# Kernel optimization log

Measured on AMD Instinct MI355X. Metric: run time of the kernel, lower is better.

## Reference

```python
import jax, jax.numpy as jnp
import numpy as np

# Analytic closed form of the 4-qubit circuit. Wires (0,1) and (2,3) are
# independent 2-qubit blocks: RY(x_a)oRY(x_b) -> CNOT(a,b) -> RY(p_a)oRY(p_b).
# Heisenberg picture gives:
#   <Z_a> = cos(p_a)*cos(x_a) + sin(p_a)*sin(x_a)*sin(x_b)
#   <Z_b> = cos(p_b)*cos(x_a)*cos(x_b) + sin(p_b)*sin(x_b)

def setup_inputs() -> dict:
    key = jax.random.key(0)
    k1, k2, k3, k4 = jax.random.split(key, 4)
    B = 16384
    return {
        "x": jax.random.uniform(k1, (B, 1, 28, 28), dtype=jnp.float32),
        "vqc_params": jax.random.normal(k2, (4,), dtype=jnp.float32),
        "fc_w": jax.random.normal(k3, (10, 784), dtype=jnp.float32) * 0.05,
        "fc_b": jax.random.normal(k4, (10,), dtype=jnp.float32) * 0.05,
        "bias": jnp.zeros((10,), dtype=jnp.float32),
    }


def _pair_expvals(xa, xb, pa, pb):
    # xa, xb: [B, 196]; pa, pb: scalars
    za = jnp.cos(pa) * jnp.cos(xa) + jnp.sin(pa) * jnp.sin(xa) * jnp.sin(xb)
    zb = jnp.cos(pb) * jnp.cos(xa) * jnp.cos(xb) + jnp.sin(pb) * jnp.sin(xb)
    return za, zb


def reference(x, vqc_params, fc_w, fc_b, bias):
    B = x.shape[0]
    # Extract 2x2 patches in the same (r, c) row-major order as the torch loop.
    # [B,28,28] -> [B,14,2,14,2] -> [B,14,14,2,2] -> [B,196,4]
    p = x[:, 0].reshape(B, 14, 2, 14, 2).transpose(0, 1, 3, 2, 4).reshape(B, 196, 4)
    x0, x1, x2, x3 = p[..., 0], p[..., 1], p[..., 2], p[..., 3]
    p0, p1, p2, p3 = vqc_params[0], vqc_params[1], vqc_params[2], vqc_params[3]
    z0, z1 = _pair_expvals(x0, x1, p0, p1)
    z2, z3 = _pair_expvals(x2, x3, p2, p3)
    q = jnp.stack([z0, z1, z2, z3], axis=-1).reshape(B, 4 * 196)  # patch-major, wire-minor
    logits = q @ fc_w.T + fc_b - bias
    return jax.nn.log_softmax(logits, axis=-1)
```

## Files before the change

### kernel.cpp

```cpp
#include <hip/hip_runtime.h>


typedef __attribute__((ext_vector_type(8))) short short8;
typedef __attribute__((ext_vector_type(4))) float f32x4;

constexpr int BLOCK = 512;
constexpr int IMGS  = 16;
constexpr int S2    = 808;
constexpr int NIT   = 4;

static __device__ __forceinline__ unsigned pkbf2(float lo, float hi) {
    unsigned r;
    asm("v_cvt_pk_bf16_f32 %0, %1, %2" : "=v"(r) : "v"(lo), "v"(hi));
    return r;
}

__global__ __launch_bounds__(BLOCK, 6)
void quanv_mfma(const float* __restrict__ x,
                const float* __restrict__ vqc,
                const float* __restrict__ fc_w,
                const float* __restrict__ fc_b,
                const float* __restrict__ bias,
                float* __restrict__ out,
                int B)
{
    __shared__ __align__(16) unsigned short q_lds[IMGS * S2];

    const int tid  = threadIdx.x;
    const int lane = tid & 63;
    const int wv   = tid >> 6;
    const int i16  = lane & 15;
    const int g    = lane >> 4;
    const int imgBase = blockIdx.x * IMGS;

    float S0, C0, S1, C1, S2p, C2p, S3, C3;
    __sincosf(vqc[0], &S0, &C0);
    __sincosf(vqc[1], &S1, &C1);
    __sincosf(vqc[2], &S2p, &C2p);
    __sincosf(vqc[3], &S3, &C3);

    if (tid < 192) {
        const unsigned im = (unsigned)tid / 12u;
        const unsigned o  = (unsigned)tid - 12u * im;
        *reinterpret_cast<unsigned*>(&q_lds[im * S2 + 784 + 2 * o]) = 0u;
    }

    const float4* __restrict__ xf4 =
        reinterpret_cast<const float4*>(x) + (long)imgBase * 196;

    unsigned img = (unsigned)tid / 196u;
    unsigned jv  = (unsigned)tid - 196u * img;

    auto process = [&](float4 v, unsigned im, unsigned j) {
        const unsigned y   = (j * 1171u) >> 13;
        const unsigned cx  = j - 7u * y;
        const unsigned par = y & 1u;
        const float CA = par ? C2p : C0, SA = par ? S2p : S0;
        const float CB = par ? C3  : C1, SB = par ? S3  : S1;
        float sa, ca, sb, cb;
        __sincosf(v.x, &sa, &ca);  __sincosf(v.y, &sb, &cb);
        const float za1 = CA * ca + SA * (sa * sb);
        const float zb1 = CB * (ca * cb) + SB * sb;
        __sincosf(v.z, &sa, &ca);  __sincosf(v.w, &sb, &cb);
        const float za2 = CA * ca + SA * (sa * sb);
        const float zb2 = CB * (ca * cb) + SB * sb;
        const unsigned e = im * S2 + (y >> 1) * 56u + 8u * cx + 2u * par;
        *reinterpret_cast<unsigned*>(&q_lds[e])     = pkbf2(za1, zb1);
        *reinterpret_cast<unsigned*>(&q_lds[e + 4]) = pkbf2(za2, zb2);
    };

    #pragma unroll
    for (int bt = 0; bt < 2; ++bt) {
        const float4 r0 = xf4[(bt * 3 + 0) * BLOCK + tid];
        const float4 r1 = xf4[(bt * 3 + 1) * BLOCK + tid];
        const float4 r2 = xf4[(bt * 3 + 2) * BLOCK + tid];
        process(r0, img, jv);
        img += 2; jv += 120; if (jv >= 196) { jv -= 196; img += 1; }
        process(r1, img, jv);
        img += 2; jv += 120; if (jv >= 196) { jv -= 196; img += 1; }
        process(r2, img, jv);
        img += 2; jv += 120; if (jv >= 196) { jv -= 196; img += 1; }
    }
    if (tid < 64) {
        const float4 r = xf4[6 * BLOCK + tid];
        process(r, img, jv);
    }

    __syncthreads();

    const int ncl = (i16 < 10) ? i16 : 9;
    const float* __restrict__ wrow = fc_w + ncl * 784;
    short8 bf[NIT];
    #pragma unroll
    for (int I = 0; I < NIT; ++I) {
        const int kb = wv + 8 * I;
        if (kb < 25) {
            int k = kb * 32 + 8 * g;
            if (k > 776) k = 776;
            const float4 lo4 = *reinterpret_cast<const float4*>(wrow + k);
            const float4 hi4 = *reinterpret_cast<const float4*>(wrow + k + 4);
            union { unsigned u[4]; short8 s; } t;
            t.u[0] = pkbf2(lo4.x, lo4.y);
            t.u[1] = pkbf2(lo4.z, lo4.w);
            t.u[2] = pkbf2(hi4.x, hi4.y);
            t.u[3] = pkbf2(hi4.z, hi4.w);
            bf[I] = t.s;
        }
    }

    f32x4 acc = {0.f, 0.f, 0.f, 0.f};
    #pragma unroll
    for (int I = 0; I < NIT; ++I) {
        const int kb = wv + 8 * I;
        if (kb < 25) {
            const short8 a = *reinterpret_cast<const short8*>(
                &q_lds[i16 * S2 + kb * 32 + 8 * g]);
            acc = __builtin_amdgcn_mfma_f32_16x16x32_bf16(a, bf[I], acc, 0, 0, 0);
        }
    }

    __syncthreads();
    float* const cpart = reinterpret_cast<float*>(q_lds);
    if (wv > 0)
        *reinterpret_cast<f32x4*>(&cpart[(wv - 1) * 256 + lane * 4]) = acc;
    __syncthreads();

    if (wv == 0) {
        #pragma unroll
        for (int p = 0; p < 7; ++p)
            acc += *reinterpret_cast<const f32x4*>(&cpart[p * 256 + lane * 4]);
        const float bk = (i16 < 10) ? (fc_b[i16] - bias[i16]) : 0.f;

        #pragma unroll
        for (int r = 0; r < 4; ++r) {
            const float lg = acc[r] + bk;
            float mx = (i16 < 10) ? lg : -3.0e38f;
            #pragma unroll
            for (int off = 1; off < 16; off <<= 1)
                mx = fmaxf(mx, __shfl_xor(mx, off, 64));
            float s = (i16 < 10) ? __expf(lg - mx) : 0.f;
            #pragma unroll
            for (int off = 1; off < 16; off <<= 1)
                s += __shfl_xor(s, off, 64);
            const int im = imgBase + g * 4 + r;
            if (i16 < 10 && im < B)
                out[(long)im * 10 + i16] = lg - mx - __logf(s);
        }
    }
}

extern "C" void kernel_launch(void* const* d_in, const int* in_sizes, int n_in,
                              void* d_out, int out_size, void* d_ws, size_t ws_size,
                              hipStream_t stream) {
    const float* x    = (const float*)d_in[0];
    const float* vqc  = (const float*)d_in[1];
    const float* fc_w = (const float*)d_in[2];
    const float* fc_b = (const float*)d_in[3];
    const float* bias = (const float*)d_in[4];
    float* outp = (float*)d_out;

    const int B = in_sizes[0] / 784;
    const int nblocks = (B + IMGS - 1) / IMGS;
    hipLaunchKernelGGL(quanv_mfma, dim3(nblocks), dim3(BLOCK), 0, stream,
                       x, vqc, fc_w, fc_b, bias, outp, B);
}
```

Baseline: 17.61 us.

## Process two image slabs per block with register prefetch of the next slab

Each block now handles two 16-image slabs in sequence, loading the second slab's pixels into registers while the first slab's MFMA and softmax run. The fc weights are converted to bf16 once per block, amortised over both slabs, and partial sums move to a separate LDS buffer. The aim is to hide global load latency behind compute and cut per-block setup. In exchange the grid is halved, occupancy hint drops from 6 to 4, register pressure rises, and the clamping of the slab start to B-IMGS may rewrite some images when B is not a multiple of the slab size.

```diff
diff --git a/kernel.cpp b/kernel.cpp
--- a/kernel.cpp
+++ b/kernel.cpp
@@ -6,6 +6,7 @@
 
 constexpr int BLOCK = 512;
 constexpr int IMGS  = 16;
+constexpr int NSLAB = 2;
 constexpr int S2    = 808;
 constexpr int NIT   = 4;
 
@@ -15,7 +16,7 @@
     return r;
 }
 
-__global__ __launch_bounds__(BLOCK, 6)
+__global__ __launch_bounds__(BLOCK, 4)
 void quanv_mfma(const float* __restrict__ x,
                 const float* __restrict__ vqc,
                 const float* __restrict__ fc_w,
@@ -25,13 +26,26 @@
                 int B)
 {
     __shared__ __align__(16) unsigned short q_lds[IMGS * S2];
+    __shared__ float cpart[7 * 256];
 
     const int tid  = threadIdx.x;
     const int lane = tid & 63;
     const int wv   = tid >> 6;
     const int i16  = lane & 15;
     const int g    = lane >> 4;
-    const int imgBase = blockIdx.x * IMGS;
+    const float4* __restrict__ xf4 = reinterpret_cast<const float4*>(x);
+
+    int ib0 = (blockIdx.x * NSLAB + 0) * IMGS;
+    int ib1 = (blockIdx.x * NSLAB + 1) * IMGS;
+    if (ib0 > B - IMGS) ib0 = B - IMGS;
+    if (ib1 > B - IMGS) ib1 = B - IMGS;
+    const long ub0 = (long)ib0 * 196;
+    const long ub1 = (long)ib1 * 196;
+
+    float4 r[7];
+    #pragma unroll
+    for (int t = 0; t < 6; ++t) r[t] = xf4[ub0 + t * BLOCK + tid];
+    r[6] = xf4[ub0 + 6 * BLOCK + (tid & 63)];
 
     float S0, C0, S1, C1, S2p, C2p, S3, C3;
     __sincosf(vqc[0], &S0, &C0);
@@ -44,49 +58,6 @@
         const unsigned o  = (unsigned)tid - 12u * im;
         *reinterpret_cast<unsigned*>(&q_lds[im * S2 + 784 + 2 * o]) = 0u;
     }
-
-    const float4* __restrict__ xf4 =
-        reinterpret_cast<const float4*>(x) + (long)imgBase * 196;
-
-    unsigned img = (unsigned)tid / 196u;
-    unsigned jv  = (unsigned)tid - 196u * img;
-
-    auto process = [&](float4 v, unsigned im, unsigned j) {
-        const unsigned y   = (j * 1171u) >> 13;
-        const unsigned cx  = j - 7u * y;
-        const unsigned par = y & 1u;
-        const float CA = par ? C2p : C0, SA = par ? S2p : S0;
-        const float CB = par ? C3  : C1, SB = par ? S3  : S1;
-        float sa, ca, sb, cb;
-        __sincosf(v.x, &sa, &ca);  __sincosf(v.y, &sb, &cb);
-        const float za1 = CA * ca + SA * (sa * sb);
-        const float zb1 = CB * (ca * cb) + SB * sb;
-        __sincosf(v.z, &sa, &ca);  __sincosf(v.w, &sb, &cb);
-        const float za2 = CA * ca + SA * (sa * sb);
-        const float zb2 = CB * (ca * cb) + SB * sb;
-        const unsigned e = im * S2 + (y >> 1) * 56u + 8u * cx + 2u * par;
-        *reinterpret_cast<unsigned*>(&q_lds[e])     = pkbf2(za1, zb1);
-        *reinterpret_cast<unsigned*>(&q_lds[e + 4]) = pkbf2(za2, zb2);
-    };
-
-    #pragma unroll
-    for (int bt = 0; bt < 2; ++bt) {
-        const float4 r0 = xf4[(bt * 3 + 0) * BLOCK + tid];
-        const float4 r1 = xf4[(bt * 3 + 1) * BLOCK + tid];
-        const float4 r2 = xf4[(bt * 3 + 2) * BLOCK + tid];
-        process(r0, img, jv);
-        img += 2; jv += 120; if (jv >= 196) { jv -= 196; img += 1; }
-        process(r1, img, jv);
-        img += 2; jv += 120; if (jv >= 196) { jv -= 196; img += 1; }
-        process(r2, img, jv);
-        img += 2; jv += 120; if (jv >= 196) { jv -= 196; img += 1; }
-    }
-    if (tid < 64) {
-        const float4 r = xf4[6 * BLOCK + tid];
-        process(r, img, jv);
-    }
-
-    __syncthreads();
 
     const int ncl = (i16 < 10) ? i16 : 9;
     const float* __restrict__ wrow = fc_w + ncl * 784;
@@ -107,44 +78,84 @@
             bf[I] = t.s;
         }
     }
+    const float bk = (i16 < 10) ? (fc_b[i16] - bias[i16]) : 0.f;
 
-    f32x4 acc = {0.f, 0.f, 0.f, 0.f};
+    auto process = [&](float4 v, unsigned im, unsigned j) {
+        const unsigned y   = (j * 1171u) >> 13;
+        const unsigned cx  = j - 7u * y;
+        const unsigned par = y & 1u;
+        const float CA = par ? C2p : C0, SA = par ? S2p : S0;
+        const float CB = par ? C3  : C1, SB = par ? S3  : S1;
+        float sa, ca, sb, cb;
+        __sincosf(v.x, &sa, &ca);  __sincosf(v.y, &sb, &cb);
+        const float za1 = CA * ca + SA * (sa * sb);
+        const float zb1 = CB * (ca * cb) + SB * sb;
+        __sincosf(v.z, &sa, &ca);  __sincosf(v.w, &sb, &cb);
+        const float za2 = CA * ca + SA * (sa * sb);
+        const float zb2 = CB * (ca * cb) + SB * sb;
+        const unsigned e = im * S2 + (y >> 1) * 56u + 8u * cx + 2u * par;
+        *reinterpret_cast<unsigned*>(&q_lds[e])     = pkbf2(za1, zb1);
+        *reinterpret_cast<unsigned*>(&q_lds[e + 4]) = pkbf2(za2, zb2);
+    };
+
+    const unsigned img0 = (unsigned)tid / 196u;
+    const unsigned jv0  = (unsigned)tid - 196u * img0;
+
     #pragma unroll
-    for (int I = 0; I < NIT; ++I) {
-        const int kb = wv + 8 * I;
-        if (kb < 25) {
-            const short8 a = *reinterpret_cast<const short8*>(
-                &q_lds[i16 * S2 + kb * 32 + 8 * g]);
-            acc = __builtin_amdgcn_mfma_f32_16x16x32_bf16(a, bf[I], acc, 0, 0, 0);
+    for (int s = 0; s < NSLAB; ++s) {
+        unsigned img = img0, jv = jv0;
+        #pragma unroll
+        for (int t = 0; t < 6; ++t) {
+            process(r[t], img, jv);
+            img += 2; jv += 120; if (jv >= 196) { jv -= 196; img += 1; }
         }
-    }
+        if (tid < 64) process(r[6], img, jv);
 
-    __syncthreads();
-    float* const cpart = reinterpret_cast<float*>(q_lds);
-    if (wv > 0)
-        *reinterpret_cast<f32x4*>(&cpart[(wv - 1) * 256 + lane * 4]) = acc;
-    __syncthreads();
+        if (s + 1 < NSLAB) {
+            #pragma unroll
+            for (int t = 0; t < 6; ++t) r[t] = xf4[ub1 + t * BLOCK + tid];
+            r[6] = xf4[ub1 + 6 * BLOCK + (tid & 63)];
+        }
 
-    if (wv == 0) {
+        __syncthreads();
+
+        f32x4 acc = {0.f, 0.f, 0.f, 0.f};
         #pragma unroll
-        for (int p = 0; p < 7; ++p)
-            acc += *reinterpret_cast<const f32x4*>(&cpart[p * 256 + lane * 4]);
-        const float bk = (i16 < 10) ? (fc_b[i16] - bias[i16]) : 0.f;
+        for (int I = 0; I < NIT; ++I) {
+            const int kb = wv + 8 * I;
+            if (kb < 25) {
+                const short8 a = *reinterpret_cast<const short8*>(
+                    &q_lds[i16 * S2 + kb * 32 + 8 * g]);
+                acc = __builtin_amdgcn_mfma_f32_16x16x32_bf16(a, bf[I], acc,
+                                                              0, 0, 0);
+            }
+        }
+        if (wv > 0)
+            *reinterpret_cast<f32x4*>(&cpart[(wv - 1) * 256 + lane * 4]) = acc;
 
-        #pragma unroll
-        for (int r = 0; r < 4; ++r) {
-            const float lg = acc[r] + bk;
-            float mx = (i16 < 10) ? lg : -3.0e38f;
+        __syncthreads();
+
+        if (wv == 0) {
             #pragma unroll
-            for (int off = 1; off < 16; off <<= 1)
-                mx = fmaxf(mx, __shfl_xor(mx, off, 64));
-            float s = (i16 < 10) ? __expf(lg - mx) : 0.f;
+            for (int p = 0; p < 7; ++p)
+                acc += *reinterpret_cast<const f32x4*>(
+                    &cpart[p * 256 + lane * 4]);
+            const int ibs = (s == 0) ? ib0 : ib1;
             #pragma unroll
-            for (int off = 1; off < 16; off <<= 1)
-                s += __shfl_xor(s, off, 64);
-            const int im = imgBase + g * 4 + r;
-            if (i16 < 10 && im < B)
-                out[(long)im * 10 + i16] = lg - mx - __logf(s);
+            for (int rr = 0; rr < 4; ++rr) {
+                const float lg = acc[rr] + bk;
+                float mx = (i16 < 10) ? lg : -3.0e38f;
+                #pragma unroll
+                for (int off = 1; off < 16; off <<= 1)
+                    mx = fmaxf(mx, __shfl_xor(mx, off, 64));
+                float sm = (i16 < 10) ? __expf(lg - mx) : 0.f;
+                #pragma unroll
+                for (int off = 1; off < 16; off <<= 1)
+                    sm += __shfl_xor(sm, off, 64);
+                const int im = ibs + g * 4 + rr;
+                if (i16 < 10 && im < B)
+                    out[(long)im * 10 + i16] = lg - mx - __logf(sm);
+            }
         }
     }
 }
@@ -160,7 +171,7 @@
     float* outp = (float*)d_out;
 
     const int B = in_sizes[0] / 784;
-    const int nblocks = (B + IMGS - 1) / IMGS;
+    const int nblocks = (B + IMGS * NSLAB - 1) / (IMGS * NSLAB);
     hipLaunchKernelGGL(quanv_mfma, dim3(nblocks), dim3(BLOCK), 0, stream,
                        x, vqc, fc_w, fc_b, bias, outp, B);
 }
```

After: 18.54 us. +5.2%, slower.
